# Performance work log

Hardware: AMD Instinct MI355X
Metric: run time of the kernel (lower is better)

The kernel has to match this reference:

```python
import jax, jax.numpy as jnp
import numpy as np
from jax import lax

B, S, D, H, T = 128, 512, 128, 128, 20


def setup_inputs() -> dict:
    key = jax.random.key(0)
    ks = jax.random.split(key, 16)
    sc = 1.0 / np.sqrt(H)
    u = lambda k, shape: jax.random.uniform(k, shape, jnp.float32, -sc, sc)
    return {
        "inputs": jax.random.normal(ks[0], (B, S, D), jnp.float32),
        "tags": jax.random.randint(ks[1], (B, S), 0, T),
        "mask": jnp.ones((B, S), jnp.bool_),
        "w_ih_f": u(ks[2], (4 * H, D)),
        "w_hh_f": u(ks[3], (4 * H, H)),
        "b_f": u(ks[4], (4 * H,)),
        "w_ih_b": u(ks[5], (4 * H, D)),
        "w_hh_b": u(ks[6], (4 * H, H)),
        "b_b": u(ks[7], (4 * H,)),
        "w_out": u(ks[8], (T, 2 * H)),
        "b_out": u(ks[9], (T,)),
        "start_trans": jax.random.uniform(ks[10], (T,), jnp.float32, -0.1, 0.1),
        "end_trans": jax.random.uniform(ks[11], (T,), jnp.float32, -0.1, 0.1),
        "trans": jax.random.uniform(ks[12], (T, T), jnp.float32, -0.1, 0.1),
    }


def _lstm_dir(x, w_ih, w_hh, b, reverse):
    # x: [B,S,D] -> hidden states [B,S,H]
    xp = jnp.einsum('bsd,gd->bsg', x, w_ih) + b  # precomputed input gates [B,S,4H]
    if reverse:
        xp = xp[:, ::-1]
    h0 = jnp.zeros((x.shape[0], H), x.dtype)
    c0 = jnp.zeros((x.shape[0], H), x.dtype)

    def step(carry, xt):
        h, c = carry
        g = xt + h @ w_hh.T
        i, f, gg, o = jnp.split(g, 4, axis=-1)
        i, f, o = jax.nn.sigmoid(i), jax.nn.sigmoid(f), jax.nn.sigmoid(o)
        c = f * c + i * jnp.tanh(gg)
        h = o * jnp.tanh(c)
        return (h, c), h

    _, hs = lax.scan(step, (h0, c0), xp.transpose(1, 0, 2))
    hs = hs.transpose(1, 0, 2)  # [B,S,H]
    if reverse:
        hs = hs[:, ::-1]
    return hs


def _crf_nll(em, tags, mask, start_trans, end_trans, trans):
    # em: [B,S,T]; torchcrf log-likelihood, reduction='mean', negated
    b, s, t = em.shape
    maskf = mask.astype(em.dtype)
    batch = jnp.arange(b)
    # numerator: score of the gold path
    num = start_trans[tags[:, 0]] + em[batch, 0, tags[:, 0]]
    em_tag = jnp.take_along_axis(em, tags[:, :, None], axis=2)[:, :, 0]  # [B,S]
    trans_tag = trans[tags[:, :-1], tags[:, 1:]]  # [B,S-1]
    num = num + jnp.sum((trans_tag + em_tag[:, 1:]) * maskf[:, 1:], axis=1)
    seq_ends = jnp.sum(mask.astype(jnp.int32), axis=1) - 1
    num = num + end_trans[tags[batch, seq_ends]]
    # denominator: forward algorithm (logsumexp semiring) via scan
    score0 = start_trans[None, :] + em[:, 0]  # [B,T]

    def step(score, inp):
        em_t, m_t = inp
        nxt = jax.nn.logsumexp(score[:, :, None] + trans[None] + em_t[:, None, :], axis=1)
        return jnp.where(m_t[:, None], nxt, score), None

    score, _ = lax.scan(step, score0, (em[:, 1:].transpose(1, 0, 2), mask[:, 1:].T))
    den = jax.nn.logsumexp(score + end_trans[None, :], axis=1)
    return -jnp.mean(num - den)


def reference(inputs, tags, mask, w_ih_f, w_hh_f, b_f, w_ih_b, w_hh_b, b_b,
              w_out, b_out, start_trans, end_trans, trans):
    h_f = _lstm_dir(inputs, w_ih_f, w_hh_f, b_f, reverse=False)
    h_b = _lstm_dir(inputs, w_ih_b, w_hh_b, b_b, reverse=True)
    lstm_out = jnp.concatenate([h_f, h_b], axis=-1)  # [B,S,2H]
    emissions = jnp.einsum('bsh,th->bst', lstm_out, w_out) + b_out  # [B,S,T]
    return _crf_nll(emissions, tags, mask, start_trans, end_trans, trans)
```

## Files before the change

### kernel.cpp

```cpp
#include <hip/hip_runtime.h>
#include <cstdint>
#include <cstddef>

#define DEVINL __device__ __forceinline__

constexpr int Bz = 128, Sl = 512, Dm = 128, Hd = 128, NC = 1024, Tt = 20;
constexpr int Mrows = Bz * Sl;

constexpr size_t OFF_XP   = 17043456;
constexpr size_t OFF_HS   = 151261184;
constexpr size_t OFF_EM   = 184815616;
constexpr size_t OFF_PART = 190058496;

DEVINL unsigned short f2bf(float f) {
    uint32_t u = __float_as_uint(f);
    u += 0x7fffu + ((u >> 16) & 1u);
    return (unsigned short)(u >> 16);
}
DEVINL float bf2f(unsigned short h) { return __uint_as_float(((uint32_t)h) << 16); }

DEVINL float rcpf(float x) { return __builtin_amdgcn_rcpf(x); }

DEVINL void barrier_lds_only() {
    __asm__ __volatile__("s_waitcnt lgkmcnt(0)" ::: "memory");
    __builtin_amdgcn_s_barrier();
    __asm__ __volatile__("" ::: "memory");
}

template <int CTRL>
DEVINL float qperm(float v) {
    int i = __float_as_int(v);
    int r = __builtin_amdgcn_update_dpp(i, i, CTRL, 0xF, 0xF, true);
    return __int_as_float(r);
}

typedef __attribute__((ext_vector_type(8))) __bf16 bf16x8;
typedef __attribute__((ext_vector_type(4))) float f32x4;
typedef _Float16 __attribute__((ext_vector_type(2))) half2_t;
typedef _Float16 __attribute__((ext_vector_type(8))) half8_t;

DEVINL half2_t u2h2(uint32_t u) { half2_t h; __builtin_memcpy(&h, &u, 4); return h; }

__global__ __launch_bounds__(256, 2) void gemm_xp_k(
    const float* __restrict__ X, const float* __restrict__ wihf, const float* __restrict__ wihb,
    const float* __restrict__ b_f, const float* __restrict__ b_b,
    unsigned short* __restrict__ xp)
{
    __shared__ __align__(16) unsigned short As[128 * 132];
    __shared__ __align__(16) unsigned short Bs[128 * 132];
    const int m0 = blockIdx.x * 128;
    const int tid = threadIdx.x;
    const int wave = tid >> 6, lane = tid & 63;
    const int wm = wave * 32;
    const int ln = lane & 15, qd = lane >> 4;
    const int colc = (tid & 31) * 4, rowb = tid >> 5;

    #pragma unroll
    for (int r = 0; r < 16; ++r) {
        int row = rowb + r * 8;
        float4 av = *(const float4*)(&X[(size_t)(m0 + row) * 128 + colc]);
        ushort4 au; au.x = f2bf(av.x); au.y = f2bf(av.y); au.z = f2bf(av.z); au.w = f2bf(av.w);
        *(ushort4*)(&As[row * 132 + colc]) = au;
    }

    const int bidx = m0 >> 9;
    const int tbase = m0 & 511;

    for (int nt = 0; nt < 8; ++nt) {
        const float* Bsrc = (nt < 4) ? (wihf + (size_t)nt * 128 * 128)
                                     : (wihb + (size_t)(nt - 4) * 128 * 128);
        __syncthreads();
        #pragma unroll
        for (int r = 0; r < 16; ++r) {
            int row = rowb + r * 8;
            float4 bv = *(const float4*)(&Bsrc[(size_t)row * 128 + colc]);
            ushort4 bu; bu.x = f2bf(bv.x); bu.y = f2bf(bv.y); bu.z = f2bf(bv.z); bu.w = f2bf(bv.w);
            *(ushort4*)(&Bs[row * 132 + colc]) = bu;
        }
        __syncthreads();

        f32x4 acc[2][8] = {};
        #pragma unroll
        for (int kk = 0; kk < 4; ++kk) {
            const int kb = kk * 32 + qd * 8;
            bf16x8 af[2], bfr[8];
            #pragma unroll
            for (int i = 0; i < 2; ++i)
                af[i] = *(const bf16x8*)(&As[(wm + i * 16 + ln) * 132 + kb]);
            #pragma unroll
            for (int j = 0; j < 8; ++j)
                bfr[j] = *(const bf16x8*)(&Bs[(j * 16 + ln) * 132 + kb]);
            #pragma unroll
            for (int i = 0; i < 2; ++i)
                #pragma unroll
                for (int j = 0; j < 8; ++j)
                    acc[i][j] = __builtin_amdgcn_mfma_f32_16x16x32_bf16(af[i], bfr[j], acc[i][j], 0, 0, 0);
        }
        #pragma unroll
        for (int j = 0; j < 8; ++j) {
            const int col = nt * 128 + j * 16 + ln;
            const float bv = (col < 512) ? b_f[col] : b_b[col - 512];
            #pragma unroll
            for (int i = 0; i < 2; ++i) {
                const int tloc = tbase + wm + i * 16 + qd * 4;
                ushort4 o;
                o.x = f2bf(acc[i][j][0] + bv); o.y = f2bf(acc[i][j][1] + bv);
                o.z = f2bf(acc[i][j][2] + bv); o.w = f2bf(acc[i][j][3] + bv);
                *(ushort4*)(xp + ((size_t)bidx * 1024 + col) * 512 + tloc) = o;
            }
        }
    }
}

__global__ __launch_bounds__(512, 1) void lstm_k(
    const float* __restrict__ whf, const float* __restrict__ whb,
    const unsigned short* __restrict__ xp, unsigned short* __restrict__ hs)
{
    __shared__ __align__(16) _Float16 h_buf[2][128];
    const int dir = blockIdx.x >> 7;
    const int b   = blockIdx.x & 127;
    const int tid = threadIdx.x;
    const int lane = tid & 63;
    const int wv   = tid >> 6;
    const int q    = lane & 3;
    const int u    = wv * 16 + (lane >> 2);
    const int grow = q * 128 + u;

    const float* wsrc = dir ? whb : whf;
    uint32_t w2[4][16];
    #pragma unroll
    for (int g = 0; g < 4; ++g) {
        const float* wrow = wsrc + (size_t)(g * 128 + u) * 128 + q * 32;
        #pragma unroll
        for (int k = 0; k < 16; ++k) {
            half2_t h2v{(_Float16)wrow[2 * k], (_Float16)wrow[2 * k + 1]};
            __builtin_memcpy(&w2[g][k], &h2v, 4);
        }
    }

    const float S  = (q == 2) ? 2.f : 1.f;
    const float Aa = (q == 2) ? 2.f : 1.f;
    const float Bc = (q == 2) ? -1.f : 0.f;

    if (tid < 128) { h_buf[0][tid] = (_Float16)0.f; h_buf[1][tid] = (_Float16)0.f; }
    __syncthreads();

    const unsigned short* xrow = xp + ((size_t)b * 1024 + dir * 512 + grow) * 512;
    unsigned short* hptr = hs + (size_t)dir * Mrows * 128 + (size_t)b * Sl * 128 + u
                              + (dir ? (size_t)(Sl - 1) * 128 : 0);
    const int hstep = dir ? -128 : 128;

    float c = 0.f;
    ushort4 cur;
    {
        ushort4 r = *(const ushort4*)(xrow + (dir ? 508 : 0));
        cur = dir ? ushort4{r.w, r.z, r.y, r.x} : r;
    }

    for (int t = 0; t < Sl; t += 4) {
        #pragma unroll
        for (int g = 0; g < 4; ++g) {
            __asm__ __volatile__(""
                : "+v"(w2[g][0]), "+v"(w2[g][1]), "+v"(w2[g][2]), "+v"(w2[g][3]),
                  "+v"(w2[g][4]), "+v"(w2[g][5]), "+v"(w2[g][6]), "+v"(w2[g][7]),
                  "+v"(w2[g][8]), "+v"(w2[g][9]), "+v"(w2[g][10]), "+v"(w2[g][11]),
                  "+v"(w2[g][12]), "+v"(w2[g][13]), "+v"(w2[g][14]), "+v"(w2[g][15]));
        }
        const int tn = (t + 4 < Sl) ? (t + 4) : 0;
        ushort4 nraw = *(const ushort4*)(xrow + (dir ? (508 - tn) : tn));

        #pragma unroll
        for (int s = 0; s < 4; ++s) {
            const int p = s & 1;
            const unsigned short xb = (s == 0) ? cur.x : (s == 1) ? cur.y : (s == 2) ? cur.z : cur.w;
            float xv = bf2f(xb);

            const half8_t* hp = (const half8_t*)&h_buf[p][q * 32];
            float p0 = 0.f, p1 = 0.f, p2 = 0.f, p3 = 0.f;
            #pragma unroll
            for (int k = 0; k < 4; ++k) {
                half8_t hv = hp[k];
                const half2_t* h2 = (const half2_t*)&hv;
                #pragma unroll
                for (int j = 0; j < 4; ++j) {
                    p0 = __builtin_amdgcn_fdot2(u2h2(w2[0][4 * k + j]), h2[j], p0, false);
                    p1 = __builtin_amdgcn_fdot2(u2h2(w2[1][4 * k + j]), h2[j], p1, false);
                    p2 = __builtin_amdgcn_fdot2(u2h2(w2[2][4 * k + j]), h2[j], p2, false);
                    p3 = __builtin_amdgcn_fdot2(u2h2(w2[3][4 * k + j]), h2[j], p3, false);
                }
            }
            float keep0 = (q & 1) ? p1 : p0;
            float send0 = (q & 1) ? p0 : p1;
            float keep1 = (q & 1) ? p3 : p2;
            float send1 = (q & 1) ? p2 : p3;
            float s0 = keep0 + qperm<0xB1>(send0);
            float s1 = keep1 + qperm<0xB1>(send1);
            float keep2 = (q & 2) ? s1 : s0;
            float send2 = (q & 2) ? s0 : s1;
            float tot = keep2 + qperm<0x4E>(send2) + xv;

            float act = Aa * rcpf(1.f + __expf(-S * tot)) + Bc;
            float a0 = qperm<0x00>(act);
            float a1 = qperm<0x55>(act);
            float a2 = qperm<0xAA>(act);
            float a3 = qperm<0xFF>(act);
            c = fmaf(a1, c, a0 * a2);
            float th = 1.f - 2.f * rcpf(1.f + __expf(2.f * c));
            float h = a3 * th;
            if (q == 0) {
                _Float16 hh = (_Float16)h;
                h_buf[1 - p][u] = hh;
                unsigned short hbits; __builtin_memcpy(&hbits, &hh, 2);
                *hptr = hbits;
            }
            hptr += hstep;
            barrier_lds_only();
        }
        cur = dir ? ushort4{nraw.w, nraw.z, nraw.y, nraw.x} : nraw;
    }
}

__global__ __launch_bounds__(320, 1) void emis_k(
    const unsigned short* __restrict__ hs, const float* __restrict__ wout,
    const float* __restrict__ bout, float* __restrict__ em)
{
    __shared__ __align__(16) half2_t wlds[20 * 128];
    const int b  = blockIdx.x >> 2;
    const int qt = blockIdx.x & 3;
    const int tid = threadIdx.x;

    #pragma unroll
    for (int k = 0; k < 8; ++k) {
        int i = tid + k * 320;
        wlds[i] = half2_t{(_Float16)wout[2 * i], (_Float16)wout[2 * i + 1]};
    }
    __syncthreads();

    const int tag  = tid % 20;
    const int copy = tid / 20;
    half2_t wreg[128];
    {
        const uint4* wl4 = (const uint4*)&wlds[tag * 128];
        #pragma unroll
        for (int k = 0; k < 32; ++k) {
            uint4 v = wl4[k];
            __builtin_memcpy(&wreg[4 * k], &v, 16);
        }
    }
    const float bo = bout[tag];
    const unsigned short* hf_base = hs + (size_t)b * Sl * 128;
    const unsigned short* hb_base = hs + (size_t)Mrows * 128 + (size_t)b * Sl * 128;

    #pragma unroll
    for (int i = 0; i < 8; ++i) {
        const int t = qt * 128 + copy + 16 * i;
        const uint4* hf4 = (const uint4*)(hf_base + (size_t)t * 128);
        const uint4* hb4 = (const uint4*)(hb_base + (size_t)t * 128);
        float a0 = bo, a1 = 0.f, a2 = 0.f, a3 = 0.f;
        #pragma unroll
        for (int k = 0; k < 16; ++k) {
            uint4 v = hf4[k];
            half2_t h2[4]; __builtin_memcpy(h2, &v, 16);
            a0 = __builtin_amdgcn_fdot2(wreg[4 * k + 0], h2[0], a0, false);
            a1 = __builtin_amdgcn_fdot2(wreg[4 * k + 1], h2[1], a1, false);
            a2 = __builtin_amdgcn_fdot2(wreg[4 * k + 2], h2[2], a2, false);
            a3 = __builtin_amdgcn_fdot2(wreg[4 * k + 3], h2[3], a3, false);
        }
        #pragma unroll
        for (int k = 0; k < 16; ++k) {
            uint4 v = hb4[k];
            half2_t h2[4]; __builtin_memcpy(h2, &v, 16);
            a0 = __builtin_amdgcn_fdot2(wreg[64 + 4 * k + 0], h2[0], a0, false);
            a1 = __builtin_amdgcn_fdot2(wreg[64 + 4 * k + 1], h2[1], a1, false);
            a2 = __builtin_amdgcn_fdot2(wreg[64 + 4 * k + 2], h2[2], a2, false);
            a3 = __builtin_amdgcn_fdot2(wreg[64 + 4 * k + 3], h2[3], a3, false);
        }
        em[((size_t)b * Sl + t) * Tt + tag] = (a0 + a1) + (a2 + a3);
    }
}

__global__ __launch_bounds__(64) void crf_k(
    const float* __restrict__ em, const int* __restrict__ tags,
    const float* __restrict__ st, const float* __restrict__ et,
    const float* __restrict__ trans, float* __restrict__ part)
{
    const int b = blockIdx.x, lane = threadIdx.x;
    const float* emb = em + (size_t)b * Sl * Tt;
    const int* tg = tags + (size_t)b * Sl;

    float nacc = 0.f;
    for (int t = 1 + lane; t < Sl; t += 64) {
        int tp = tg[t - 1], tc = tg[t];
        nacc += trans[tp * Tt + tc] + emb[t * Tt + tc];
    }
    #pragma unroll
    for (int off = 32; off; off >>= 1) nacc += __shfl_down(nacc, off);

    float Etr[20];
    #pragma unroll
    for (int i = 0; i < 20; ++i)
        Etr[i] = (lane < 20) ? __expf(trans[i * Tt + lane]) : 0.f;

    float C = 0.f;
    float p = (lane < 20) ? __expf(st[lane] + emb[lane]) : 0.f;

    float evr[8];
    #pragma unroll
    for (int s = 0; s < 8; ++s) {
        int tt = 1 + s; tt = tt < Sl ? tt : Sl - 1;
        evr[s] = (lane < 20) ? emb[(size_t)tt * Tt + lane] : 0.f;
    }

    for (int t0 = 1; t0 < Sl; t0 += 8) {
        #pragma unroll
        for (int s = 0; s < 8; ++s) {
            const int t = t0 + s;
            if (t < Sl) {
                float ev = evr[s];
                int tf = t + 8; tf = tf < Sl ? tf : Sl - 1;
                evr[s] = (lane < 20) ? emb[(size_t)tf * Tt + lane] : 0.f;

                float q0 = 0.f, q1 = 0.f, q2 = 0.f, q3 = 0.f;
                #pragma unroll
                for (int i = 0; i < 20; i += 4) {
                    q0 = fmaf(__int_as_float(__builtin_amdgcn_readlane(__float_as_int(p), i + 0)), Etr[i + 0], q0);
                    q1 = fmaf(__int_as_float(__builtin_amdgcn_readlane(__float_as_int(p), i + 1)), Etr[i + 1], q1);
                    q2 = fmaf(__int_as_float(__builtin_amdgcn_readlane(__float_as_int(p), i + 2)), Etr[i + 2], q2);
                    q3 = fmaf(__int_as_float(__builtin_amdgcn_readlane(__float_as_int(p), i + 3)), Etr[i + 3], q3);
                }
                p = ((q0 + q1) + (q2 + q3)) * __expf(ev);
                if ((s & 3) == 3) {
                    float S0 = 0.f, S1 = 0.f, S2 = 0.f, S3 = 0.f;
                    #pragma unroll
                    for (int i = 0; i < 20; i += 4) {
                        S0 += __int_as_float(__builtin_amdgcn_readlane(__float_as_int(p), i + 0));
                        S1 += __int_as_float(__builtin_amdgcn_readlane(__float_as_int(p), i + 1));
                        S2 += __int_as_float(__builtin_amdgcn_readlane(__float_as_int(p), i + 2));
                        S3 += __int_as_float(__builtin_amdgcn_readlane(__float_as_int(p), i + 3));
                    }
                    float Ssum = (S0 + S1) + (S2 + S3);
                    C += __logf(Ssum);
                    p *= rcpf(Ssum);
                }
            }
        }
    }
    float f = (lane < 20) ? p * __expf(et[lane]) : 0.f;
    float S0 = 0.f, S1 = 0.f, S2 = 0.f, S3 = 0.f;
    #pragma unroll
    for (int i = 0; i < 20; i += 4) {
        S0 += __int_as_float(__builtin_amdgcn_readlane(__float_as_int(f), i + 0));
        S1 += __int_as_float(__builtin_amdgcn_readlane(__float_as_int(f), i + 1));
        S2 += __int_as_float(__builtin_amdgcn_readlane(__float_as_int(f), i + 2));
        S3 += __int_as_float(__builtin_amdgcn_readlane(__float_as_int(f), i + 3));
    }
    float den = C + __logf((S0 + S1) + (S2 + S3));
    if (lane == 0)
        part[b] = nacc + st[tg[0]] + emb[tg[0]] + et[tg[Sl - 1]] - den;
}

__global__ void fin_k(const float* __restrict__ part, float* __restrict__ out) {
    int l = threadIdx.x;
    float v = part[l] + part[l + 64];
    #pragma unroll
    for (int off = 32; off; off >>= 1) v += __shfl_xor(v, off);
    if (l == 0) out[0] = -v * (1.f / 128.f);
}

extern "C" void kernel_launch(void* const* d_in, const int* in_sizes, int n_in,
                              void* d_out, int out_size, void* d_ws, size_t ws_size,
                              hipStream_t stream) {
    const float* x      = (const float*)d_in[0];
    const int*   tags   = (const int*)d_in[1];
    const float* w_ih_f = (const float*)d_in[3];
    const float* w_hh_f = (const float*)d_in[4];
    const float* b_f    = (const float*)d_in[5];
    const float* w_ih_b = (const float*)d_in[6];
    const float* w_hh_b = (const float*)d_in[7];
    const float* b_b    = (const float*)d_in[8];
    const float* w_out  = (const float*)d_in[9];
    const float* b_out  = (const float*)d_in[10];
    const float* st     = (const float*)d_in[11];
    const float* et     = (const float*)d_in[12];
    const float* trans  = (const float*)d_in[13];
    float* out = (float*)d_out;

    char* ws = (char*)d_ws;
    unsigned short* xp   = (unsigned short*)(ws + OFF_XP);
    unsigned short* hs   = (unsigned short*)(ws + OFF_HS);
    float*          em   = (float*)(ws + OFF_EM);
    float*          part = (float*)(ws + OFF_PART);

    gemm_xp_k<<<Mrows / 128, 256, 0, stream>>>(x, w_ih_f, w_ih_b, b_f, b_b, xp);
    lstm_k<<<256, 512, 0, stream>>>(w_hh_f, w_hh_b, xp, hs);
    emis_k<<<Bz * 4, 320, 0, stream>>>(hs, w_out, b_out, em);
    crf_k<<<Bz, 64, 0, stream>>>(em, tags, st, et, trans, part);
    fin_k<<<1, 64, 0, stream>>>(part, out);
}
```

Before: 515.5 us.

## Use MFMA 16x16x32 f16 for LSTM recurrent matvec instead of fdot2

Replaces the per-lane fdot2 recurrent matvec with quad DPP reductions by MFMA 16x16x32 f16 instructions. The hidden vector is broadcast across the A operand and weights are held as B fragments. Each lane now computes all four gates for its unit directly, so the cross-lane permutes are no longer needed. The matrix unit wastes 15 of 16 rows, since batch is 1 per block, and MFMA latency now sits on the serial recurrence critical path.

Measured after the change: 499.9 us. 1.03x faster.

```diff
diff --git a/kernel.cpp b/kernel.cpp
--- a/kernel.cpp
+++ b/kernel.cpp
@@ -27,19 +27,10 @@
     __asm__ __volatile__("" ::: "memory");
 }
 
-template <int CTRL>
-DEVINL float qperm(float v) {
-    int i = __float_as_int(v);
-    int r = __builtin_amdgcn_update_dpp(i, i, CTRL, 0xF, 0xF, true);
-    return __int_as_float(r);
-}
-
 typedef __attribute__((ext_vector_type(8))) __bf16 bf16x8;
 typedef __attribute__((ext_vector_type(4))) float f32x4;
 typedef _Float16 __attribute__((ext_vector_type(2))) half2_t;
 typedef _Float16 __attribute__((ext_vector_type(8))) half8_t;
-
-DEVINL half2_t u2h2(uint32_t u) { half2_t h; __builtin_memcpy(&h, &u, 4); return h; }
 
 __global__ __launch_bounds__(256, 2) void gemm_xp_k(
     const float* __restrict__ X, const float* __restrict__ wihf, const float* __restrict__ wihb,
@@ -122,92 +113,108 @@
     const int tid = threadIdx.x;
     const int lane = tid & 63;
     const int wv   = tid >> 6;
-    const int q    = lane & 3;
-    const int u    = wv * 16 + (lane >> 2);
-    const int grow = q * 128 + u;
+    const int ln   = lane & 15;
+    const int qd   = lane >> 4;
+    const int u    = wv * 16 + ln;
 
     const float* wsrc = dir ? whb : whf;
-    uint32_t w2[4][16];
-    #pragma unroll
-    for (int g = 0; g < 4; ++g) {
-        const float* wrow = wsrc + (size_t)(g * 128 + u) * 128 + q * 32;
-        #pragma unroll
-        for (int k = 0; k < 16; ++k) {
-            half2_t h2v{(_Float16)wrow[2 * k], (_Float16)wrow[2 * k + 1]};
-            __builtin_memcpy(&w2[g][k], &h2v, 4);
-        }
-    }
-
-    const float S  = (q == 2) ? 2.f : 1.f;
-    const float Aa = (q == 2) ? 2.f : 1.f;
-    const float Bc = (q == 2) ? -1.f : 0.f;
+    half8_t wfr[4][4];
+    #pragma unroll
+    for (int j = 0; j < 4; ++j) {
+        const float* wrow = wsrc + (size_t)(j * 128 + u) * 128;
+        #pragma unroll
+        for (int kk = 0; kk < 4; ++kk) {
+            float4 v0 = *(const float4*)(wrow + kk * 32 + qd * 8);
+            float4 v1 = *(const float4*)(wrow + kk * 32 + qd * 8 + 4);
+            half8_t hv;
+            hv[0] = (_Float16)v0.x; hv[1] = (_Float16)v0.y;
+            hv[2] = (_Float16)v0.z; hv[3] = (_Float16)v0.w;
+            hv[4] = (_Float16)v1.x; hv[5] = (_Float16)v1.y;
+            hv[6] = (_Float16)v1.z; hv[7] = (_Float16)v1.w;
+            wfr[j][kk] = hv;
+        }
+    }
 
     if (tid < 128) { h_buf[0][tid] = (_Float16)0.f; h_buf[1][tid] = (_Float16)0.f; }
     __syncthreads();
 
-    const unsigned short* xrow = xp + ((size_t)b * 1024 + dir * 512 + grow) * 512;
+    const unsigned short* xr0 = xp + ((size_t)b * 1024 + (size_t)dir * 512 + u) * 512;
+    const unsigned short* xr1 = xr0 + (size_t)128 * 512;
+    const unsigned short* xr2 = xr0 + (size_t)256 * 512;
+    const unsigned short* xr3 = xr0 + (size_t)384 * 512;
+
     unsigned short* hptr = hs + (size_t)dir * Mrows * 128 + (size_t)b * Sl * 128 + u
                               + (dir ? (size_t)(Sl - 1) * 128 : 0);
     const int hstep = dir ? -128 : 128;
 
     float c = 0.f;
-    ushort4 cur;
+    ushort4 cur0, cur1, cur2, cur3;
     {
-        ushort4 r = *(const ushort4*)(xrow + (dir ? 508 : 0));
-        cur = dir ? ushort4{r.w, r.z, r.y, r.x} : r;
+        const int o0 = dir ? 508 : 0;
+        ushort4 r0 = *(const ushort4*)(xr0 + o0);
+        ushort4 r1 = *(const ushort4*)(xr1 + o0);
+        ushort4 r2 = *(const ushort4*)(xr2 + o0);
+        ushort4 r3 = *(const ushort4*)(xr3 + o0);
+        cur0 = dir ? ushort4{r0.w, r0.z, r0.y, r0.x} : r0;
+        cur1 = dir ? ushort4{r1.w, r1.z, r1.y, r1.x} : r1;
+        cur2 = dir ? ushort4{r2.w, r2.z, r2.y, r2.x} : r2;
+        cur3 = dir ? ushort4{r3.w, r3.z, r3.y, r3.x} : r3;
     }
 
     for (int t = 0; t < Sl; t += 4) {
-        #pragma unroll
-        for (int g = 0; g < 4; ++g) {
-            __asm__ __volatile__(""
-                : "+v"(w2[g][0]), "+v"(w2[g][1]), "+v"(w2[g][2]), "+v"(w2[g][3]),
-                  "+v"(w2[g][4]), "+v"(w2[g][5]), "+v"(w2[g][6]), "+v"(w2[g][7]),
-                  "+v"(w2[g][8]), "+v"(w2[g][9]), "+v"(w2[g][10]), "+v"(w2[g][11]),
-                  "+v"(w2[g][12]), "+v"(w2[g][13]), "+v"(w2[g][14]), "+v"(w2[g][15]));
-        }
         const int tn = (t + 4 < Sl) ? (t + 4) : 0;
-        ushort4 nraw = *(const ushort4*)(xrow + (dir ? (508 - tn) : tn));
+        const int on = dir ? (508 - tn) : tn;
+        ushort4 n0 = *(const ushort4*)(xr0 + on);
+        ushort4 n1 = *(const ushort4*)(xr1 + on);
+        ushort4 n2 = *(const ushort4*)(xr2 + on);
+        ushort4 n3 = *(const ushort4*)(xr3 + on);
 
         #pragma unroll
         for (int s = 0; s < 4; ++s) {
             const int p = s & 1;
-            const unsigned short xb = (s == 0) ? cur.x : (s == 1) ? cur.y : (s == 2) ? cur.z : cur.w;
-            float xv = bf2f(xb);
-
-            const half8_t* hp = (const half8_t*)&h_buf[p][q * 32];
-            float p0 = 0.f, p1 = 0.f, p2 = 0.f, p3 = 0.f;
-            #pragma unroll
-            for (int k = 0; k < 4; ++k) {
-                half8_t hv = hp[k];
-                const half2_t* h2 = (const half2_t*)&hv;
-                #pragma unroll
-                for (int j = 0; j < 4; ++j) {
-                    p0 = __builtin_amdgcn_fdot2(u2h2(w2[0][4 * k + j]), h2[j], p0, false);
-                    p1 = __builtin_amdgcn_fdot2(u2h2(w2[1][4 * k + j]), h2[j], p1, false);
-                    p2 = __builtin_amdgcn_fdot2(u2h2(w2[2][4 * k + j]), h2[j], p2, false);
-                    p3 = __builtin_amdgcn_fdot2(u2h2(w2[3][4 * k + j]), h2[j], p3, false);
-                }
-            }
-            float keep0 = (q & 1) ? p1 : p0;
-            float send0 = (q & 1) ? p0 : p1;
-            float keep1 = (q & 1) ? p3 : p2;
-            float send1 = (q & 1) ? p2 : p3;
-            float s0 = keep0 + qperm<0xB1>(send0);
-            float s1 = keep1 + qperm<0xB1>(send1);
-            float keep2 = (q & 2) ? s1 : s0;
-            float send2 = (q & 2) ? s0 : s1;
-            float tot = keep2 + qperm<0x4E>(send2) + xv;
-
-            float act = Aa * rcpf(1.f + __expf(-S * tot)) + Bc;
-            float a0 = qperm<0x00>(act);
-            float a1 = qperm<0x55>(act);
-            float a2 = qperm<0xAA>(act);
-            float a3 = qperm<0xFF>(act);
-            c = fmaf(a1, c, a0 * a2);
+            const half8_t* hb = (const half8_t*)&h_buf[p][0];
+            half8_t a0 = hb[qd];
+            half8_t a1 = hb[4 + qd];
+            half8_t a2 = hb[8 + qd];
+            half8_t a3 = hb[12 + qd];
+
+            f32x4 ac0 = {}, ac1 = {}, ac2 = {}, ac3 = {};
+            ac0 = __builtin_amdgcn_mfma_f32_16x16x32_f16(a0, wfr[0][0], ac0, 0, 0, 0);
+            ac1 = __builtin_amdgcn_mfma_f32_16x16x32_f16(a0, wfr[1][0], ac1, 0, 0, 0);
+            ac2 = __builtin_amdgcn_mfma_f32_16x16x32_f16(a0, wfr[2][0], ac2, 0, 0, 0);
+            ac3 = __builtin_amdgcn_mfma_f32_16x16x32_f16(a0, wfr[3][0], ac3, 0, 0, 0);
+            ac0 = __builtin_amdgcn_mfma_f32_16x16x32_f16(a1, wfr[0][1], ac0, 0, 0, 0);
+            ac1 = __builtin_amdgcn_mfma_f32_16x16x32_f16(a1, wfr[1][1], ac1, 0, 0, 0);
+            ac2 = __builtin_amdgcn_mfma_f32_16x16x32_f16(a1, wfr[2][1], ac2, 0, 0, 0);
+            ac3 = __builtin_amdgcn_mfma_f32_16x16x32_f16(a1, wfr[3][1], ac3, 0, 0, 0);
+            ac0 = __builtin_amdgcn_mfma_f32_16x16x32_f16(a2, wfr[0][2], ac0, 0, 0, 0);
+            ac1 = __builtin_amdgcn_mfma_f32_16x16x32_f16(a2, wfr[1][2], ac1, 0, 0, 0);
+            ac2 = __builtin_amdgcn_mfma_f32_16x16x32_f16(a2, wfr[2][2], ac2, 0, 0, 0);
+            ac3 = __builtin_amdgcn_mfma_f32_16x16x32_f16(a2, wfr[3][2], ac3, 0, 0, 0);
+            ac0 = __builtin_amdgcn_mfma_f32_16x16x32_f16(a3, wfr[0][3], ac0, 0, 0, 0);
+            ac1 = __builtin_amdgcn_mfma_f32_16x16x32_f16(a3, wfr[1][3], ac1, 0, 0, 0);
+            ac2 = __builtin_amdgcn_mfma_f32_16x16x32_f16(a3, wfr[2][3], ac2, 0, 0, 0);
+            ac3 = __builtin_amdgcn_mfma_f32_16x16x32_f16(a3, wfr[3][3], ac3, 0, 0, 0);
+
+            const unsigned short xb0 = (s == 0) ? cur0.x : (s == 1) ? cur0.y : (s == 2) ? cur0.z : cur0.w;
+            const unsigned short xb1 = (s == 0) ? cur1.x : (s == 1) ? cur1.y : (s == 2) ? cur1.z : cur1.w;
+            const unsigned short xb2 = (s == 0) ? cur2.x : (s == 1) ? cur2.y : (s == 2) ? cur2.z : cur2.w;
+            const unsigned short xb3 = (s == 0) ? cur3.x : (s == 1) ? cur3.y : (s == 2) ? cur3.z : cur3.w;
+
+            float t0 = ac0[0] + bf2f(xb0);
+            float t1 = ac1[0] + bf2f(xb1);
+            float t2 = ac2[0] + bf2f(xb2);
+            float t3 = ac3[0] + bf2f(xb3);
+
+            float gi = rcpf(1.f + __expf(-t0));
+            float gf = rcpf(1.f + __expf(-t1));
+            float gg = 2.f * rcpf(1.f + __expf(-2.f * t2)) - 1.f;
+            float go = rcpf(1.f + __expf(-t3));
+            c = fmaf(gf, c, gi * gg);
             float th = 1.f - 2.f * rcpf(1.f + __expf(2.f * c));
-            float h = a3 * th;
-            if (q == 0) {
+            float h = go * th;
+
+            if (qd == 0) {
                 _Float16 hh = (_Float16)h;
                 h_buf[1 - p][u] = hh;
                 unsigned short hbits; __builtin_memcpy(&hbits, &hh, 2);
@@ -216,7 +223,10 @@
             hptr += hstep;
             barrier_lds_only();
         }
-        cur = dir ? ushort4{nraw.w, nraw.z, nraw.y, nraw.x} : nraw;
+        cur0 = dir ? ushort4{n0.w, n0.z, n0.y, n0.x} : n0;
+        cur1 = dir ? ushort4{n1.w, n1.z, n1.y, n1.x} : n1;
+        cur2 = dir ? ushort4{n2.w, n2.z, n2.y, n2.x} : n2;
+        cur3 = dir ? ushort4{n3.w, n3.z, n3.y, n3.x} : n3;
     }
 }
 
```
